# Optimization experiments

Measured on AMD Instinct MI355X. Metric: run time of the kernel, lower is better.

The kernel has to match this reference:

```python
import jax, jax.numpy as jnp
import numpy as np

N_HEADS = 8
N_HEAD_CH = 32
N_GROUPS = 8
NC = N_HEADS * N_HEAD_CH          # 256
GC = NC // N_GROUPS               # 32 group channels
OFFSET_RANGE_FACTOR = 2.0


def _layer_norm(x, w, b, eps=1e-5):
    mu = jnp.mean(x, -1, keepdims=True)
    var = jnp.var(x, -1, keepdims=True)
    return (x - mu) * jax.lax.rsqrt(var + eps) * w + b


def _conv2dmod(x, style, W):
    # StyleGAN2-style modulated 1x1 conv (lucidrains Conv2DMod, demod=True).
    # x (B,Ci,H,W), style (B,Ci), W (Co,Ci)
    w = W[None] * (style[:, None, :] + 1.0)                      # (B,Co,Ci)
    d = jax.lax.rsqrt(jnp.sum(w * w, axis=2, keepdims=True) + 1e-8)
    w = w * d
    return jnp.einsum('boi,bihw->bohw', w, x)


def _dwconv3x3(x, w, b):
    # depthwise 3x3, stride 1, pad 1; w (C,1,3,3)
    out = jax.lax.conv_general_dilated(
        x, w, window_strides=(1, 1), padding=[(1, 1), (1, 1)],
        dimension_numbers=('NCHW', 'OIHW', 'NCHW'),
        feature_group_count=x.shape[1])
    return out + b[None, :, None, None]


def _grid_sample(img, grid):
    # bilinear, align_corners=True, padding_mode='zeros'
    # img (N,C,H,W), grid (N,Hg,Wg,2) in xy order, values in ~[-1,1]
    N, C, H, W = img.shape
    gx = (grid[..., 0] + 1.0) * 0.5 * (W - 1)
    gy = (grid[..., 1] + 1.0) * 0.5 * (H - 1)
    x0 = jnp.floor(gx); y0 = jnp.floor(gy)
    wx1 = gx - x0; wy1 = gy - y0

    def gather(ix, iy):
        valid = ((ix >= 0) & (ix <= W - 1) & (iy >= 0) & (iy <= H - 1)).astype(img.dtype)
        ixc = jnp.clip(ix, 0, W - 1).astype(jnp.int32)
        iyc = jnp.clip(iy, 0, H - 1).astype(jnp.int32)
        vals = jax.vmap(lambda im, yy, xx: im[:, yy, xx])(img, iyc, ixc)  # (N,C,Hg,Wg)
        return vals * valid[:, None]

    x1 = x0 + 1.0; y1 = y0 + 1.0
    return (gather(x0, y0) * ((1 - wx1) * (1 - wy1))[:, None]
            + gather(x1, y0) * (wx1 * (1 - wy1))[:, None]
            + gather(x0, y1) * ((1 - wx1) * wy1)[:, None]
            + gather(x1, y1) * (wx1 * wy1)[:, None])


def _ref_points(Hk, Wk, BG, dtype):
    ry = jnp.linspace(0.5, Hk - 0.5, Hk, dtype=dtype) / (Hk - 1.0) * 2.0 - 1.0
    rx = jnp.linspace(0.5, Wk - 0.5, Wk, dtype=dtype) / (Wk - 1.0) * 2.0 - 1.0
    ref = jnp.stack(jnp.meshgrid(ry, rx, indexing='ij'), -1)  # (Hk,Wk,2) yx
    return jnp.broadcast_to(ref[None], (BG, Hk, Wk, 2))


def setup_inputs() -> dict:
    key = jax.random.key(0)
    ks = jax.random.split(key, 16)
    s = 0.02
    inp = {
        'x': jax.random.normal(ks[0], (2, NC, 32, 32), jnp.float32),
        'q': jax.random.normal(ks[1], (8, 2048, NC), jnp.float32),
        'mask': (jax.random.uniform(ks[2], (8, 2048, 1)) > 0.2).astype(jnp.float32),
        'Wq': jax.random.normal(ks[3], (NC, NC), jnp.float32) * s,
        'bq': jnp.zeros((NC,), jnp.float32),
        'Wmod': jax.random.normal(ks[4], (NC, NC), jnp.float32),
        'dw_w': jax.random.normal(ks[5], (GC, 1, 3, 3), jnp.float32) * s,
        'dw_b': jnp.zeros((GC,), jnp.float32),
        'ln_w': jnp.ones((GC,), jnp.float32),
        'ln_b': jnp.zeros((GC,), jnp.float32),
        'off_w': jax.random.normal(ks[6], (2, GC), jnp.float32) * s,
        'Wk': jax.random.normal(ks[7], (NC, NC), jnp.float32) * s,
        'bk': jnp.zeros((NC,), jnp.float32),
        'Wv': jax.random.normal(ks[8], (NC, NC), jnp.float32) * s,
        'bv': jnp.zeros((NC,), jnp.float32),
        'Wo': jax.random.normal(ks[9], (NC, NC), jnp.float32) * s,
        'bo': jnp.zeros((NC,), jnp.float32),
    }
    return inp


def reference(x, q, mask, Wq, bq, Wmod, dw_w, dw_b, ln_w, ln_b, off_w,
              Wk, bk, Wv, bv, Wo, bo):
    rn = q.shape[0] // x.shape[0]
    B, L, C = q.shape
    H, W = x.shape[2], x.shape[3]

    # masked mean pooling of queries -> conditioning vector
    q_cond = jnp.sum(q * mask, axis=1) / (jnp.sum(mask, axis=1) + 1e-6)   # (B,C)
    q_cond = q_cond @ Wq.T + bq

    # tile reference features: 'ref_n c h w -> (rn ref_n) c h w'
    xr = jnp.tile(x, (rn, 1, 1, 1))                                       # (B,C,H,W)

    # modulated 1x1 conv, then per-group offset network
    q_t = _conv2dmod(xr, q_cond, Wmod)                                    # (B,C,H,W)
    q_off = q_t.reshape(B * N_GROUPS, GC, H, W)
    t = _dwconv3x3(q_off, dw_w, dw_b)
    t = jnp.transpose(t, (0, 2, 3, 1))
    t = _layer_norm(t, ln_w, ln_b)
    t = jax.nn.gelu(t, approximate=False)
    t = jnp.transpose(t, (0, 3, 1, 2))
    offset = jnp.einsum('oi,bihw->bohw', off_w, t)                        # (BG,2,Hk,Wk)

    Hk, Wk_ = offset.shape[2], offset.shape[3]
    n_sample = Hk * Wk_
    offset_range = jnp.array([1.0 / (Hk - 1.0), 1.0 / (Wk_ - 1.0)],
                             dtype=x.dtype).reshape(1, 2, 1, 1)
    offset = jnp.tanh(offset) * offset_range * OFFSET_RANGE_FACTOR
    offset = jnp.transpose(offset, (0, 2, 3, 1))                          # (BG,Hk,Wk,2) yx

    ref = _ref_points(Hk, Wk_, B * N_GROUPS, x.dtype)
    pos = offset + ref                                                    # no clamp (orf>=0)

    # deformable gather
    xs = _grid_sample(xr.reshape(B * N_GROUPS, GC, H, W), pos[..., ::-1]) # (BG,GC,Hk,Wk)
    xs = xs.reshape(B, C, 1, n_sample)

    k = (jnp.einsum('oi,bimn->bomn', Wk, xs) + bk[None, :, None, None]
         ).reshape(B * N_HEADS, N_HEAD_CH, n_sample)
    v = (jnp.einsum('oi,bimn->bomn', Wv, xs) + bv[None, :, None, None]
         ).reshape(B * N_HEADS, N_HEAD_CH, n_sample)
    qh = jnp.transpose(q, (0, 2, 1)).reshape(B * N_HEADS, N_HEAD_CH, L)

    scale = N_HEAD_CH ** (-0.5)
    attn = jnp.einsum('bcm,bcn->bmn', qh, k) * scale                      # (BH,L,ns)
    # NOTE: source's attn.masked_fill(...) is non-in-place and discarded -> no mask here
    attn = jax.nn.softmax(attn, axis=2)
    out = jnp.einsum('bmn,bcn->bcm', attn, v)                             # (BH,hc,L)

    # '(b gn) c l -> b l (gn c)' with gn = n_groups (== n_heads)
    out = out.reshape(B, N_GROUPS, N_HEAD_CH, L).transpose(0, 3, 1, 2).reshape(B, L, NC)
    y = out @ Wo.T + bo
    return (y,
            pos.reshape(B, N_GROUPS, Hk, Wk_, 2),
            ref.reshape(B, N_GROUPS, Hk, Wk_, 2))
```

## Files before the change

kernel.cpp:

```cpp
#include <hip/hip_runtime.h>
#include <math.h>

typedef unsigned int uint;
typedef unsigned short ushort;
typedef __attribute__((ext_vector_type(8))) short short8;
typedef __attribute__((ext_vector_type(4))) float f32x4;

constexpr int CB  = 8;
constexpr int CL  = 2048;
constexpr int CC  = 256;
constexpr int CHC = 32;
constexpr int CGC = 32;
constexpr int CHW = 1024;
constexpr int CNS = 1024;
constexpr int CBG = 64;

constexpr size_t WS_QCOND = 2176;
constexpr size_t WS_WMOD  = 4224;
constexpr size_t WS_XT    = 266368;
constexpr size_t WS_QT    = 528512;
constexpr size_t WS_XST   = 2756736;
constexpr size_t WS_KB    = 3805312;
constexpr size_t WS_VB    = 4853888;
constexpr size_t WS_WB    = 5902464;
constexpr size_t WS_TMPB  = 6000768;
constexpr size_t WS_QB    = 8097920;
constexpr size_t WS_PART  = 10195072;
constexpr size_t WS_MPART = 10260608;

static __device__ __forceinline__ ushort f2bf(float f) {
  uint u = __float_as_uint(f);
  return (ushort)((u + 0x7FFFu + ((u >> 16) & 1u)) >> 16);
}
static __device__ __forceinline__ float bf2f(ushort u) {
  return __uint_as_float((uint)u << 16);
}
static __device__ __forceinline__ uint pack2bf(float a, float b) {
  return (uint)f2bf(a) | ((uint)f2bf(b) << 16);
}
static __device__ __forceinline__ uint packtrunc(float lo, float hi) {
  return __builtin_amdgcn_perm(__float_as_uint(hi), __float_as_uint(lo), 0x07060302u);
}

__global__ void k_pool(const float* __restrict__ q, const float* __restrict__ mask,
                       float* __restrict__ part, float* __restrict__ mpart,
                       ushort* __restrict__ qb) {
  int b  = blockIdx.x >> 5;
  int lc = blockIdx.x & 31;
  int l0 = lc * 64;
  int tid = threadIdx.x;
  const float scale = 0.17677669529663687f * 1.4426950408889634f;
  __shared__ float mloc[64];
  if (tid < 64) mloc[tid] = mask[b * CL + l0 + tid];
  __syncthreads();
  if (tid == 0) {
    float s = 0.f;
    for (int j = 0; j < 64; j++) s += mloc[j];
    mpart[b * 32 + lc] = s;
  }
  float acc = 0.f;
  const float* qp = q + (size_t)(b * CL + l0) * CC + tid;
  ushort* qw = qb + (size_t)(b * CL + l0) * CC + tid;
  for (int j = 0; j < 64; j++) {
    float v = qp[(size_t)j * CC];
    acc += v * mloc[j];
    qw[(size_t)j * CC] = f2bf(v * scale);
  }
  part[((size_t)(b * 32 + lc)) * CC + tid] = acc;
}

__global__ void k_qcond(const float* __restrict__ part, const float* __restrict__ mpart,
                        const float* __restrict__ Wq, const float* __restrict__ bq,
                        float* __restrict__ qcond) {
  int b = blockIdx.x, o = threadIdx.x;
  __shared__ float qm[CC];
  __shared__ float ms;
  float s = 0.f;
  const float* pp = part + (size_t)b * 32 * CC + o;
  #pragma unroll
  for (int lc = 0; lc < 32; lc++) s += pp[(size_t)lc * CC];
  if (o < 32) {
    float m = mpart[b * 32 + o];
    #pragma unroll
    for (int k = 1; k < 32; k <<= 1) m += __shfl_xor(m, k, 32);
    if (o == 0) ms = m;
  }
  __syncthreads();
  float inv = 1.f / (ms + 1e-6f);
  qm[o] = s * inv;
  __syncthreads();
  float acc = bq[o];
  const float* wrow = Wq + (size_t)o * CC;
  for (int i = 0; i < CC; i++) acc += wrow[i] * qm[i];
  qcond[b * CC + o] = acc;
}

__global__ void k_wprep(const float* __restrict__ Wmod, const float* __restrict__ qcond,
                        ushort* __restrict__ wmodb) {
  int b  = blockIdx.x >> 4;
  int og = blockIdx.x & 15;
  int tid = threadIdx.x;
  int ol = tid >> 4, seg = tid & 15;
  int o = og * 16 + ol;
  const float* wr = Wmod + (size_t)o * CC + seg * 16;
  const float* qc = qcond + b * CC + seg * 16;
  float m[16];
  float ss = 0.f;
  #pragma unroll
  for (int j = 0; j < 16; j++) {
    float v = wr[j] * (qc[j] + 1.f);
    m[j] = v;
    ss += v * v;
  }
  #pragma unroll
  for (int k = 1; k < 16; k <<= 1) ss += __shfl_xor(ss, k, 16);
  float d = rsqrtf(ss + 1e-8f);
  uint u[8];
  #pragma unroll
  for (int j = 0; j < 8; j++) u[j] = pack2bf(m[2 * j] * d, m[2 * j + 1] * d);
  ushort* dst = wmodb + ((size_t)(b * CC + o)) * CC + seg * 16;
  *(uint4*)(dst)     = make_uint4(u[0], u[1], u[2], u[3]);
  *(uint4*)(dst + 8) = make_uint4(u[4], u[5], u[6], u[7]);
}

__global__ void k_prep(const float* __restrict__ x, const float* __restrict__ Wk,
                       const float* __restrict__ Wv, const float* __restrict__ Wo,
                       ushort* __restrict__ xt, ushort* __restrict__ wb) {
  int bid = blockIdx.x;
  int tid = threadIdx.x;
  if (bid < 128) {
    int ref  = bid >> 6;
    int cblk = (bid >> 4) & 3;
    int hwblk = bid & 15;
    __shared__ float t[64][65];
    int c0 = cblk * 64, hw0 = hwblk * 64;
    const float* src = x + (size_t)ref * CC * CHW;
    int hl = tid & 63, cq = tid >> 6;
    #pragma unroll
    for (int r = 0; r < 16; r++) {
      int cl = cq * 16 + r;
      t[cl][hl] = src[(size_t)(c0 + cl) * CHW + hw0 + hl];
    }
    __syncthreads();
    int cl2 = tid & 63, hq = tid >> 6;
    #pragma unroll
    for (int r = 0; r < 16; r++) {
      int hwl = hq * 16 + r;
      xt[((size_t)(ref * CHW + hw0 + hwl)) * CC + c0 + cl2] = f2bf(t[cl2][hwl]);
    }
  } else {
    int t = (bid - 128) * 256 + tid;
    int which = t >> 13;
    size_t off = ((size_t)(t & 8191)) * 8;
    const float* src = (which == 0) ? Wk : (which == 1) ? Wv : Wo;
    float4 a = *(const float4*)(src + off);
    float4 b = *(const float4*)(src + off + 4);
    uint4 r;
    r.x = pack2bf(a.x, a.y); r.y = pack2bf(a.z, a.w);
    r.z = pack2bf(b.x, b.y); r.w = pack2bf(b.z, b.w);
    *(uint4*)(wb + (size_t)which * 65536 + off) = r;
  }
}

__launch_bounds__(256)
__global__ void k_mod_mfma(const ushort* __restrict__ wmodb, const ushort* __restrict__ xt,
                           float* __restrict__ qt) {
  int tid = threadIdx.x;
  int wid = tid >> 6, lane = tid & 63;
  int widx = blockIdx.x * 4 + wid;
  int b   = widx >> 10;
  int ot  = (widx >> 6) & 15;
  int hwt = widx & 63;
  int col = lane & 15, g = lane >> 4;
  int O0 = ot * 16, HW0 = hwt * 16;
  const ushort* ap = wmodb + ((size_t)(b * CC + O0 + col)) * CC + g * 8;
  const ushort* bp = xt + ((size_t)((b & 1) * CHW + HW0 + col)) * CC + g * 8;
  f32x4 acc = {0.f, 0.f, 0.f, 0.f};
  #pragma unroll
  for (int ks = 0; ks < 8; ks++) {
    short8 af = *(const short8*)(ap + ks * 32);
    short8 bf = *(const short8*)(bp + ks * 32);
    acc = __builtin_amdgcn_mfma_f32_16x16x32_bf16(af, bf, acc, 0, 0, 0);
  }
  float4 st;
  st.x = acc[0]; st.y = acc[1]; st.z = acc[2]; st.w = acc[3];
  *(float4*)(qt + ((size_t)(b * CHW + HW0 + col)) * CC + O0 + g * 4) = st;
}

__global__ void k_off_sample(const float* __restrict__ qt, const float* __restrict__ dww,
                             const float* __restrict__ dwb, const float* __restrict__ lnw,
                             const float* __restrict__ lnb, const float* __restrict__ offw,
                             const ushort* __restrict__ xt,
                             float* __restrict__ out_pos, float* __restrict__ out_ref,
                             ushort* __restrict__ xst) {
  int bg   = blockIdx.x >> 7;
  int pblk = blockIdx.x & 127;
  int tid  = threadIdx.x;
  int c = tid & 31, pp = tid >> 5;
  int p0 = pblk * 8;
  int yy = p0 >> 5;
  int xx = (p0 & 31) + pp;
  int p  = p0 + pp;
  const float* src = qt + ((size_t)(bg >> 3) * CHW) * CC + (bg & 7) * CGC + c;
  float acc = dwb[c];
  #pragma unroll
  for (int ky = 0; ky < 3; ky++) {
    int yr = yy + ky - 1;
    if (yr < 0 || yr > 31) continue;
    #pragma unroll
    for (int kx = 0; kx < 3; kx++) {
      int xc = xx + kx - 1;
      if (xc < 0 || xc > 31) continue;
      acc += dww[c * 9 + ky * 3 + kx] * src[(size_t)(yr * 32 + xc) * CC];
    }
  }
  float s1 = acc, s2 = acc * acc;
  #pragma unroll
  for (int m = 1; m < 32; m <<= 1) { s1 += __shfl_xor(s1, m, 32); s2 += __shfl_xor(s2, m, 32); }
  float mu  = s1 * (1.f / 32.f);
  float var = s2 * (1.f / 32.f) - mu * mu;
  float tn  = (acc - mu) * rsqrtf(var + 1e-5f) * lnw[c] + lnb[c];
  float g   = 0.5f * tn * (1.f + erff(tn * 0.70710678118654752f));
  float sy = offw[c] * g, sx = offw[32 + c] * g;
  #pragma unroll
  for (int m = 1; m < 32; m <<= 1) { sy += __shfl_xor(sy, m, 32); sx += __shfl_xor(sx, m, 32); }

  float mine  = tanhf((c & 1) ? sx : sy);
  float other = __shfl_xor(mine, 1, 32);
  float ty = (c & 1) ? other : mine;
  float tx = (c & 1) ? mine : other;

  float refy = (0.5f + (float)yy) * (2.f / 31.f) - 1.f;
  float refx = (0.5f + (float)xx) * (2.f / 31.f) - 1.f;
  float py = ty * (2.f / 31.f) + refy;
  float px = tx * (2.f / 31.f) + refx;
  if (c < 2) {
    int oidx = bg * 2048 + p * 2 + c;
    out_pos[oidx] = (c == 0) ? py : px;
    out_ref[oidx] = (c == 0) ? refy : refx;
  }

  float gx = (px + 1.f) * 15.5f;
  float gy = (py + 1.f) * 15.5f;
  float x0f = floorf(gx), y0f = floorf(gy);
  float wx = gx - x0f, wy = gy - y0f;
  int ix0 = (int)x0f, iy0 = (int)y0f;
  const ushort* img = xt + (size_t)(((bg >> 3) & 1)) * CHW * CC + (bg & 7) * CGC + c;
  float sacc = 0.f;
  #pragma unroll
  for (int dy = 0; dy < 2; dy++) {
    int iy = iy0 + dy;
    if (iy < 0 || iy > 31) continue;
    float wyv = dy ? wy : 1.f - wy;
    #pragma unroll
    for (int dx = 0; dx < 2; dx++) {
      int ix = ix0 + dx;
      if (ix < 0 || ix > 31) continue;
      float wxv = dx ? wx : 1.f - wx;
      sacc += wyv * wxv * bf2f(img[(size_t)(iy * 32 + ix) * CC]);
    }
  }
  xst[((size_t)((bg >> 3) * CNS) + p) * CC + (bg & 7) * CGC + c] = f2bf(sacc);
}

__launch_bounds__(256)
__global__ void k_kv_mfma(const ushort* __restrict__ xst, const ushort* __restrict__ wkb,
                          const ushort* __restrict__ wvb, const float* __restrict__ bk,
                          const float* __restrict__ bv, ushort* __restrict__ kb,
                          ushort* __restrict__ vb) {
  int tid = threadIdx.x;
  int wid = tid >> 6, lane = tid & 63;
  int widx = blockIdx.x * 4 + wid;
  int b   = widx >> 8;
  int ntg = (widx >> 3) & 31;
  int otg = widx & 7;
  int col = lane & 15, g = lane >> 4;
  int N0 = ntg * 32, O0 = otg * 32;

  const ushort* xs0 = xst + ((size_t)(b * CNS + N0 + col)) * CC + g * 8;
  const ushort* xs1 = xs0 + (size_t)16 * CC;
  const ushort* wk0 = wkb + (size_t)(O0 + col) * CC + g * 8;
  const ushort* wk1 = wk0 + (size_t)16 * CC;
  const ushort* wv0 = wvb + (size_t)(O0 + col) * CC + g * 8;
  const ushort* wv1 = wv0 + (size_t)16 * CC;

  f32x4 ka[2][2], va[2][2];
  #pragma unroll
  for (int Y = 0; Y < 2; Y++) {
    float bvv = bv[O0 + Y * 16 + col];
    #pragma unroll
    for (int r = 0; r < 4; r++) {
      float bkv = bk[O0 + Y * 16 + g * 4 + r];
      ka[0][Y][r] = bkv; ka[1][Y][r] = bkv;
      va[0][Y][r] = bvv; va[1][Y][r] = bvv;
    }
  }

  #pragma unroll
  for (int ks = 0; ks < 8; ks++) {
    short8 xf0 = *(const short8*)(xs0 + ks * 32);
    short8 xf1 = *(const short8*)(xs1 + ks * 32);
    short8 kf0 = *(const short8*)(wk0 + ks * 32);
    short8 kf1 = *(const short8*)(wk1 + ks * 32);
    short8 vf0 = *(const short8*)(wv0 + ks * 32);
    short8 vf1 = *(const short8*)(wv1 + ks * 32);
    ka[0][0] = __builtin_amdgcn_mfma_f32_16x16x32_bf16(kf0, xf0, ka[0][0], 0, 0, 0);
    ka[0][1] = __builtin_amdgcn_mfma_f32_16x16x32_bf16(kf1, xf0, ka[0][1], 0, 0, 0);
    ka[1][0] = __builtin_amdgcn_mfma_f32_16x16x32_bf16(kf0, xf1, ka[1][0], 0, 0, 0);
    ka[1][1] = __builtin_amdgcn_mfma_f32_16x16x32_bf16(kf1, xf1, ka[1][1], 0, 0, 0);
    va[0][0] = __builtin_amdgcn_mfma_f32_16x16x32_bf16(xf0, vf0, va[0][0], 0, 0, 0);
    va[0][1] = __builtin_amdgcn_mfma_f32_16x16x32_bf16(xf0, vf1, va[0][1], 0, 0, 0);
    va[1][0] = __builtin_amdgcn_mfma_f32_16x16x32_bf16(xf1, vf0, va[1][0], 0, 0, 0);
    va[1][1] = __builtin_amdgcn_mfma_f32_16x16x32_bf16(xf1, vf1, va[1][1], 0, 0, 0);
  }

  #pragma unroll
  for (int X = 0; X < 2; X++)
    #pragma unroll
    for (int Y = 0; Y < 2; Y++) {
      int Oy = O0 + Y * 16, Nx = N0 + X * 16;
      {
        int hh = Oy >> 5;
        int c0 = (Oy & 31) + g * 4;
        uint2 w;
        w.x = pack2bf(ka[X][Y][0], ka[X][Y][1]);
        w.y = pack2bf(ka[X][Y][2], ka[X][Y][3]);
        *(uint2*)(kb + ((size_t)((b * 8 + hh) * CNS + Nx + col)) * CHC + c0) = w;
      }
      {
        int o = Oy + col;
        int hh = o >> 5;
        uint2 w;
        w.x = pack2bf(va[X][Y][0], va[X][Y][1]);
        w.y = pack2bf(va[X][Y][2], va[X][Y][3]);
        *(uint2*)(vb + ((size_t)((b * 8 + hh) * CHC + (o & 31))) * CNS + Nx + g * 4) = w;
      }
    }
}

__launch_bounds__(512, 4)
__global__ void k_attn_mfma(const ushort* __restrict__ qb, const ushort* __restrict__ kb,
                            const ushort* __restrict__ vb, ushort* __restrict__ tmpb) {
  int bh = blockIdx.x >> 3;
  int mb = blockIdx.x & 7;
  int b = bh >> 3, h = bh & 7;
  int tid = threadIdx.x;
  int wid = tid >> 6, lane = tid & 63;
  int col = lane & 15, g = lane >> 4;
  int mA = mb * 256 + wid * 32 + col;

  __shared__ ushort Kst[2][64 * 40];
  __shared__ ushort Vst[2][32 * 72];
  __shared__ ushort plds[8][2048];

  char* pwA = (char*)&plds[wid][0];
  char* pwB = (char*)&plds[wid][1024];
  int swz = (col & 7) << 4;
  int wb0 = col * 128 + g * 8;
  int rb0 = (col * 128 + g * 16) ^ swz;
  int rb1 = (col * 128 + 64 + g * 16) ^ swz;

  const ushort* qpA = qb + ((size_t)(b * CL + mA)) * CC + h * CHC + g * 8;
  short8 qfA = *(const short8*)qpA;
  short8 qfB = *(const short8*)(qpA + 16 * CC);

  const ushort* kglob = kb + (size_t)bh * 32768 + tid * 4;
  const ushort* vglob = vb + (size_t)bh * 32768 + (tid >> 4) * 1024 + (tid & 15) * 4;
  int kdst = (tid >> 3) * 40 + (tid & 7) * 4;
  int vdst = (tid >> 4) * 72 + (tid & 15) * 4;

  f32x4 oA0 = {0.f,0.f,0.f,0.f}, oA1 = {0.f,0.f,0.f,0.f};
  f32x4 oB0 = {0.f,0.f,0.f,0.f}, oB1 = {0.f,0.f,0.f,0.f};
  float lA = 0.f, lB = 0.f;

  {
    uint2 kx = *(const uint2*)(kglob);
    uint2 vx = *(const uint2*)(vglob);
    *(uint2*)&Kst[0][kdst] = kx;
    *(uint2*)&Vst[0][vdst] = vx;
  }
  __syncthreads();

  int cur = 0;
  for (int ch = 0; ch < 16; ch++) {
    uint2 kx, vx;
    if (ch < 15) {
      kx = *(const uint2*)(kglob + (ch + 1) * 2048);
      vx = *(const uint2*)(vglob + (ch + 1) * 64);
    }

    const ushort* Kc = &Kst[cur][0];
    const ushort* Vc = &Vst[cur][0];
    short8 kf0 = *(const short8*)(Kc + ( 0 + col) * 40 + g * 8);
    short8 kf1 = *(const short8*)(Kc + (16 + col) * 40 + g * 8);
    short8 kf2 = *(const short8*)(Kc + (32 + col) * 40 + g * 8);
    short8 kf3 = *(const short8*)(Kc + (48 + col) * 40 + g * 8);
    short8 vf00 = *(const short8*)(Vc + (col     ) * 72 +  0 + g * 8);
    short8 vf01 = *(const short8*)(Vc + (col     ) * 72 + 32 + g * 8);
    short8 vf10 = *(const short8*)(Vc + (col + 16) * 72 +  0 + g * 8);
    short8 vf11 = *(const short8*)(Vc + (col + 16) * 72 + 32 + g * 8);

    f32x4 zero = {0.f,0.f,0.f,0.f};
    f32x4 sA0 = __builtin_amdgcn_mfma_f32_16x16x32_bf16(kf0, qfA, zero, 0, 0, 0);
    f32x4 sA1 = __builtin_amdgcn_mfma_f32_16x16x32_bf16(kf1, qfA, zero, 0, 0, 0);
    f32x4 sA2 = __builtin_amdgcn_mfma_f32_16x16x32_bf16(kf2, qfA, zero, 0, 0, 0);
    f32x4 sA3 = __builtin_amdgcn_mfma_f32_16x16x32_bf16(kf3, qfA, zero, 0, 0, 0);
    f32x4 sB0 = __builtin_amdgcn_mfma_f32_16x16x32_bf16(kf0, qfB, zero, 0, 0, 0);
    f32x4 sB1 = __builtin_amdgcn_mfma_f32_16x16x32_bf16(kf1, qfB, zero, 0, 0, 0);
    f32x4 sB2 = __builtin_amdgcn_mfma_f32_16x16x32_bf16(kf2, qfB, zero, 0, 0, 0);
    f32x4 sB3 = __builtin_amdgcn_mfma_f32_16x16x32_bf16(kf3, qfB, zero, 0, 0, 0);

    {
      float ps = 0.f;
      #pragma unroll
      for (int f = 0; f < 4; f++) {
        f32x4 s = (f == 0) ? sA0 : (f == 1) ? sA1 : (f == 2) ? sA2 : sA3;
        float p0 = __builtin_amdgcn_exp2f(s[0]);
        float p1 = __builtin_amdgcn_exp2f(s[1]);
        float p2 = __builtin_amdgcn_exp2f(s[2]);
        float p3 = __builtin_amdgcn_exp2f(s[3]);
        ps += (p0 + p1) + (p2 + p3);
        *(uint2*)(pwA + ((wb0 + f * 32) ^ swz)) = make_uint2(packtrunc(p0, p1), packtrunc(p2, p3));
      }
      lA += ps;
    }
    {
      float ps = 0.f;
      #pragma unroll
      for (int f = 0; f < 4; f++) {
        f32x4 s = (f == 0) ? sB0 : (f == 1) ? sB1 : (f == 2) ? sB2 : sB3;
        float p0 = __builtin_amdgcn_exp2f(s[0]);
        float p1 = __builtin_amdgcn_exp2f(s[1]);
        float p2 = __builtin_amdgcn_exp2f(s[2]);
        float p3 = __builtin_amdgcn_exp2f(s[3]);
        ps += (p0 + p1) + (p2 + p3);
        *(uint2*)(pwB + ((wb0 + f * 32) ^ swz)) = make_uint2(packtrunc(p0, p1), packtrunc(p2, p3));
      }
      lB += ps;
    }

    short8 pfA0 = *(const short8*)(pwA + rb0);
    short8 pfA1 = *(const short8*)(pwA + rb1);
    short8 pfB0 = *(const short8*)(pwB + rb0);
    short8 pfB1 = *(const short8*)(pwB + rb1);

    oA0 = __builtin_amdgcn_mfma_f32_16x16x32_bf16(vf00, pfA0, oA0, 0, 0, 0);
    oA0 = __builtin_amdgcn_mfma_f32_16x16x32_bf16(vf01, pfA1, oA0, 0, 0, 0);
    oA1 = __builtin_amdgcn_mfma_f32_16x16x32_bf16(vf10, pfA0, oA1, 0, 0, 0);
    oA1 = __builtin_amdgcn_mfma_f32_16x16x32_bf16(vf11, pfA1, oA1, 0, 0, 0);
    oB0 = __builtin_amdgcn_mfma_f32_16x16x32_bf16(vf00, pfB0, oB0, 0, 0, 0);
    oB0 = __builtin_amdgcn_mfma_f32_16x16x32_bf16(vf01, pfB1, oB0, 0, 0, 0);
    oB1 = __builtin_amdgcn_mfma_f32_16x16x32_bf16(vf10, pfB0, oB1, 0, 0, 0);
    oB1 = __builtin_amdgcn_mfma_f32_16x16x32_bf16(vf11, pfB1, oB1, 0, 0, 0);

    if (ch < 15) {
      *(uint2*)&Kst[cur ^ 1][kdst] = kx;
      *(uint2*)&Vst[cur ^ 1][vdst] = vx;
    }
    __syncthreads();
    cur ^= 1;
  }

  lA += __shfl_xor(lA, 16); lA += __shfl_xor(lA, 32);
  lB += __shfl_xor(lB, 16); lB += __shfl_xor(lB, 32);
  float rlA = 1.f / lA, rlB = 1.f / lB;

  ushort* opA = tmpb + ((size_t)(b * CL + mA)) * CC + h * CHC;
  ushort* opB = opA + 16 * CC;
  {
    uint2 w0, w1;
    w0.x = pack2bf(oA0[0] * rlA, oA0[1] * rlA);
    w0.y = pack2bf(oA0[2] * rlA, oA0[3] * rlA);
    w1.x = pack2bf(oA1[0] * rlA, oA1[1] * rlA);
    w1.y = pack2bf(oA1[2] * rlA, oA1[3] * rlA);
    *(uint2*)(opA + g * 4) = w0;
    *(uint2*)(opA + 16 + g * 4) = w1;
  }
  {
    uint2 w0, w1;
    w0.x = pack2bf(oB0[0] * rlB, oB0[1] * rlB);
    w0.y = pack2bf(oB0[2] * rlB, oB0[3] * rlB);
    w1.x = pack2bf(oB1[0] * rlB, oB1[1] * rlB);
    w1.y = pack2bf(oB1[2] * rlB, oB1[3] * rlB);
    *(uint2*)(opB + g * 4) = w0;
    *(uint2*)(opB + 16 + g * 4) = w1;
  }
}

__launch_bounds__(256)
__global__ void k_yproj_mfma(const ushort* __restrict__ tmpb, const ushort* __restrict__ wob,
                             const float* __restrict__ bo, float* __restrict__ y) {
  int tid = threadIdx.x;
  int wid = tid >> 6, lane = tid & 63;
  int widx = blockIdx.x * 4 + wid;
  int rt2 = widx >> 1;
  int og = widx & 1;
  int col = lane & 15, g = lane >> 4;
  int R0 = rt2 * 32, O0 = og * 128;

  const ushort* ap0 = tmpb + ((size_t)(R0 + col)) * CC + g * 8;
  const ushort* ap1 = ap0 + (size_t)16 * CC;
  const ushort* bp = wob + (size_t)(O0 + col) * CC + g * 8;

  f32x4 acc[2][8];
  #pragma unroll
  for (int o4 = 0; o4 < 8; o4++) {
    float bb = bo[O0 + o4 * 16 + col];
    #pragma unroll
    for (int r = 0; r < 4; r++) { acc[0][o4][r] = bb; acc[1][o4][r] = bb; }
  }

  #pragma unroll
  for (int ks = 0; ks < 8; ks++) {
    short8 af0 = *(const short8*)(ap0 + ks * 32);
    short8 af1 = *(const short8*)(ap1 + ks * 32);
    #pragma unroll
    for (int o4 = 0; o4 < 8; o4++) {
      short8 bf = *(const short8*)(bp + (size_t)o4 * 16 * CC + ks * 32);
      acc[0][o4] = __builtin_amdgcn_mfma_f32_16x16x32_bf16(af0, bf, acc[0][o4], 0, 0, 0);
      acc[1][o4] = __builtin_amdgcn_mfma_f32_16x16x32_bf16(af1, bf, acc[1][o4], 0, 0, 0);
    }
  }

  #pragma unroll
  for (int rr = 0; rr < 2; rr++)
    #pragma unroll
    for (int o4 = 0; o4 < 8; o4++)
      #pragma unroll
      for (int r = 0; r < 4; r++)
        y[(size_t)(R0 + rr * 16 + g * 4 + r) * CC + O0 + o4 * 16 + col] = acc[rr][o4][r];
}

extern "C" void kernel_launch(void* const* d_in, const int* in_sizes, int n_in,
                              void* d_out, int out_size, void* d_ws, size_t ws_size,
                              hipStream_t stream) {
  const float* x    = (const float*)d_in[0];
  const float* q    = (const float*)d_in[1];
  const float* mask = (const float*)d_in[2];
  const float* Wq   = (const float*)d_in[3];
  const float* bq   = (const float*)d_in[4];
  const float* Wmod = (const float*)d_in[5];
  const float* dw_w = (const float*)d_in[6];
  const float* dw_b = (const float*)d_in[7];
  const float* ln_w = (const float*)d_in[8];
  const float* ln_b = (const float*)d_in[9];
  const float* offw = (const float*)d_in[10];
  const float* Wk   = (const float*)d_in[11];
  const float* bk   = (const float*)d_in[12];
  const float* Wv   = (const float*)d_in[13];
  const float* bv   = (const float*)d_in[14];
  const float* Wo   = (const float*)d_in[15];
  const float* bo   = (const float*)d_in[16];

  float* ws = (float*)d_ws;
  float* out = (float*)d_out;
  float* out_y   = out;
  float* out_pos = out + (size_t)CB * CL * CC;
  float* out_ref = out_pos + (size_t)CBG * CHW * 2;

  ushort* wmodb = (ushort*)(ws + WS_WMOD);
  ushort* xt    = (ushort*)(ws + WS_XT);
  float*  qt    = ws + WS_QT;
  ushort* xst   = (ushort*)(ws + WS_XST);
  ushort* kbuf  = (ushort*)(ws + WS_KB);
  ushort* vbuf  = (ushort*)(ws + WS_VB);
  ushort* wkb   = (ushort*)(ws + WS_WB);
  ushort* wvb   = wkb + 65536;
  ushort* wob   = wkb + 131072;
  ushort* tmpb  = (ushort*)(ws + WS_TMPB);
  ushort* qbuf  = (ushort*)(ws + WS_QB);
  float*  part  = ws + WS_PART;
  float*  mpart = ws + WS_MPART;

  k_pool<<<256, 256, 0, stream>>>(q, mask, part, mpart, qbuf);
  k_qcond<<<8, 256, 0, stream>>>(part, mpart, Wq, bq, ws + WS_QCOND);
  k_prep<<<224, 256, 0, stream>>>(x, Wk, Wv, Wo, xt, wkb);
  k_wprep<<<128, 256, 0, stream>>>(Wmod, ws + WS_QCOND, wmodb);
  k_mod_mfma<<<2048, 256, 0, stream>>>(wmodb, xt, qt);
  k_off_sample<<<8192, 256, 0, stream>>>(qt, dw_w, dw_b, ln_w, ln_b, offw, xt,
                                         out_pos, out_ref, xst);
  k_kv_mfma<<<512, 256, 0, stream>>>(xst, wkb, wvb, bk, bv, kbuf, vbuf);
  k_attn_mfma<<<512, 512, 0, stream>>>(qbuf, kbuf, vbuf, tmpb);
  k_yproj_mfma<<<256, 256, 0, stream>>>(tmpb, wob, bo, out_y);
}
```

Measured before the change: 132.0 us.

## Merge pool and prep kernels, store qt as bf16, double attention chunk size

```diff
diff --git a/kernel.cpp b/kernel.cpp
--- a/kernel.cpp
+++ b/kernel.cpp
@@ -42,31 +42,70 @@
   return __builtin_amdgcn_perm(__float_as_uint(hi), __float_as_uint(lo), 0x07060302u);
 }
 
-__global__ void k_pool(const float* __restrict__ q, const float* __restrict__ mask,
-                       float* __restrict__ part, float* __restrict__ mpart,
-                       ushort* __restrict__ qb) {
-  int b  = blockIdx.x >> 5;
-  int lc = blockIdx.x & 31;
-  int l0 = lc * 64;
+__global__ void k_poolprep(const float* __restrict__ q, const float* __restrict__ mask,
+                           float* __restrict__ part, float* __restrict__ mpart,
+                           ushort* __restrict__ qb,
+                           const float* __restrict__ x, const float* __restrict__ Wk,
+                           const float* __restrict__ Wv, const float* __restrict__ Wo,
+                           ushort* __restrict__ xt, ushort* __restrict__ wb) {
+  int bid = blockIdx.x;
   int tid = threadIdx.x;
-  const float scale = 0.17677669529663687f * 1.4426950408889634f;
-  __shared__ float mloc[64];
-  if (tid < 64) mloc[tid] = mask[b * CL + l0 + tid];
-  __syncthreads();
-  if (tid == 0) {
-    float s = 0.f;
-    for (int j = 0; j < 64; j++) s += mloc[j];
-    mpart[b * 32 + lc] = s;
-  }
-  float acc = 0.f;
-  const float* qp = q + (size_t)(b * CL + l0) * CC + tid;
-  ushort* qw = qb + (size_t)(b * CL + l0) * CC + tid;
-  for (int j = 0; j < 64; j++) {
-    float v = qp[(size_t)j * CC];
-    acc += v * mloc[j];
-    qw[(size_t)j * CC] = f2bf(v * scale);
-  }
-  part[((size_t)(b * 32 + lc)) * CC + tid] = acc;
+  __shared__ float shbuf[64 * 65];
+  if (bid < 256) {
+    int b  = bid >> 5;
+    int lc = bid & 31;
+    int l0 = lc * 64;
+    const float scale = 0.17677669529663687f * 1.4426950408889634f;
+    float* mloc = shbuf;
+    if (tid < 64) mloc[tid] = mask[b * CL + l0 + tid];
+    __syncthreads();
+    if (tid == 0) {
+      float s = 0.f;
+      for (int j = 0; j < 64; j++) s += mloc[j];
+      mpart[b * 32 + lc] = s;
+    }
+    float acc = 0.f;
+    const float* qp = q + (size_t)(b * CL + l0) * CC + tid;
+    ushort* qw = qb + (size_t)(b * CL + l0) * CC + tid;
+    for (int j = 0; j < 64; j++) {
+      float v = qp[(size_t)j * CC];
+      acc += v * mloc[j];
+      qw[(size_t)j * CC] = f2bf(v * scale);
+    }
+    part[((size_t)(b * 32 + lc)) * CC + tid] = acc;
+  } else if (bid < 384) {
+    int b2 = bid - 256;
+    int ref  = b2 >> 6;
+    int cblk = (b2 >> 4) & 3;
+    int hwblk = b2 & 15;
+    float (*t)[65] = (float(*)[65])shbuf;
+    int c0 = cblk * 64, hw0 = hwblk * 64;
+    const float* src = x + (size_t)ref * CC * CHW;
+    int hl = tid & 63, cq = tid >> 6;
+    #pragma unroll
+    for (int r = 0; r < 16; r++) {
+      int cl = cq * 16 + r;
+      t[cl][hl] = src[(size_t)(c0 + cl) * CHW + hw0 + hl];
+    }
+    __syncthreads();
+    int cl2 = tid & 63, hq = tid >> 6;
+    #pragma unroll
+    for (int r = 0; r < 16; r++) {
+      int hwl = hq * 16 + r;
+      xt[((size_t)(ref * CHW + hw0 + hwl)) * CC + c0 + cl2] = f2bf(t[cl2][hwl]);
+    }
+  } else {
+    int t2 = (bid - 384) * 256 + tid;
+    int which = t2 >> 13;
+    size_t off = ((size_t)(t2 & 8191)) * 8;
+    const float* src = (which == 0) ? Wk : (which == 1) ? Wv : Wo;
+    float4 a = *(const float4*)(src + off);
+    float4 b = *(const float4*)(src + off + 4);
+    uint4 r;
+    r.x = pack2bf(a.x, a.y); r.y = pack2bf(a.z, a.w);
+    r.z = pack2bf(b.x, b.y); r.w = pack2bf(b.z, b.w);
+    *(uint4*)(wb + (size_t)which * 65536 + off) = r;
+  }
 }
 
 __global__ void k_qcond(const float* __restrict__ part, const float* __restrict__ mpart,
@@ -123,48 +162,9 @@
   *(uint4*)(dst + 8) = make_uint4(u[4], u[5], u[6], u[7]);
 }
 
-__global__ void k_prep(const float* __restrict__ x, const float* __restrict__ Wk,
-                       const float* __restrict__ Wv, const float* __restrict__ Wo,
-                       ushort* __restrict__ xt, ushort* __restrict__ wb) {
-  int bid = blockIdx.x;
-  int tid = threadIdx.x;
-  if (bid < 128) {
-    int ref  = bid >> 6;
-    int cblk = (bid >> 4) & 3;
-    int hwblk = bid & 15;
-    __shared__ float t[64][65];
-    int c0 = cblk * 64, hw0 = hwblk * 64;
-    const float* src = x + (size_t)ref * CC * CHW;
-    int hl = tid & 63, cq = tid >> 6;
-    #pragma unroll
-    for (int r = 0; r < 16; r++) {
-      int cl = cq * 16 + r;
-      t[cl][hl] = src[(size_t)(c0 + cl) * CHW + hw0 + hl];
-    }
-    __syncthreads();
-    int cl2 = tid & 63, hq = tid >> 6;
-    #pragma unroll
-    for (int r = 0; r < 16; r++) {
-      int hwl = hq * 16 + r;
-      xt[((size_t)(ref * CHW + hw0 + hwl)) * CC + c0 + cl2] = f2bf(t[cl2][hwl]);
-    }
-  } else {
-    int t = (bid - 128) * 256 + tid;
-    int which = t >> 13;
-    size_t off = ((size_t)(t & 8191)) * 8;
-    const float* src = (which == 0) ? Wk : (which == 1) ? Wv : Wo;
-    float4 a = *(const float4*)(src + off);
-    float4 b = *(const float4*)(src + off + 4);
-    uint4 r;
-    r.x = pack2bf(a.x, a.y); r.y = pack2bf(a.z, a.w);
-    r.z = pack2bf(b.x, b.y); r.w = pack2bf(b.z, b.w);
-    *(uint4*)(wb + (size_t)which * 65536 + off) = r;
-  }
-}
-
 __launch_bounds__(256)
 __global__ void k_mod_mfma(const ushort* __restrict__ wmodb, const ushort* __restrict__ xt,
-                           float* __restrict__ qt) {
+                           ushort* __restrict__ qtb) {
   int tid = threadIdx.x;
   int wid = tid >> 6, lane = tid & 63;
   int widx = blockIdx.x * 4 + wid;
@@ -182,12 +182,13 @@
     short8 bf = *(const short8*)(bp + ks * 32);
     acc = __builtin_amdgcn_mfma_f32_16x16x32_bf16(af, bf, acc, 0, 0, 0);
   }
-  float4 st;
-  st.x = acc[0]; st.y = acc[1]; st.z = acc[2]; st.w = acc[3];
-  *(float4*)(qt + ((size_t)(b * CHW + HW0 + col)) * CC + O0 + g * 4) = st;
-}
-
-__global__ void k_off_sample(const float* __restrict__ qt, const float* __restrict__ dww,
+  uint2 st;
+  st.x = pack2bf(acc[0], acc[1]);
+  st.y = pack2bf(acc[2], acc[3]);
+  *(uint2*)(qtb + ((size_t)(b * CHW + HW0 + col)) * CC + O0 + g * 4) = st;
+}
+
+__global__ void k_off_sample(const ushort* __restrict__ qtb, const float* __restrict__ dww,
                              const float* __restrict__ dwb, const float* __restrict__ lnw,
                              const float* __restrict__ lnb, const float* __restrict__ offw,
                              const ushort* __restrict__ xt,
@@ -201,7 +202,7 @@
   int yy = p0 >> 5;
   int xx = (p0 & 31) + pp;
   int p  = p0 + pp;
-  const float* src = qt + ((size_t)(bg >> 3) * CHW) * CC + (bg & 7) * CGC + c;
+  const ushort* src = qtb + ((size_t)(bg >> 3) * CHW) * CC + (bg & 7) * CGC + c;
   float acc = dwb[c];
   #pragma unroll
   for (int ky = 0; ky < 3; ky++) {
@@ -211,7 +212,7 @@
     for (int kx = 0; kx < 3; kx++) {
       int xc = xx + kx - 1;
       if (xc < 0 || xc > 31) continue;
-      acc += dww[c * 9 + ky * 3 + kx] * src[(size_t)(yr * 32 + xc) * CC];
+      acc += dww[c * 9 + ky * 3 + kx] * bf2f(src[(size_t)(yr * 32 + xc) * CC]);
     }
   }
   float s1 = acc, s2 = acc * acc;
@@ -349,8 +350,8 @@
   int col = lane & 15, g = lane >> 4;
   int mA = mb * 256 + wid * 32 + col;
 
-  __shared__ ushort Kst[2][64 * 40];
-  __shared__ ushort Vst[2][32 * 72];
+  __shared__ ushort Kst[2][2][64 * 40];
+  __shared__ ushort Vst[2][2][32 * 72];
   __shared__ ushort plds[8][2048];
 
   char* pwA = (char*)&plds[wid][0];
@@ -374,88 +375,100 @@
   float lA = 0.f, lB = 0.f;
 
   {
-    uint2 kx = *(const uint2*)(kglob);
-    uint2 vx = *(const uint2*)(vglob);
-    *(uint2*)&Kst[0][kdst] = kx;
-    *(uint2*)&Vst[0][vdst] = vx;
+    uint2 k0 = *(const uint2*)(kglob);
+    uint2 k1 = *(const uint2*)(kglob + 2048);
+    uint2 v0 = *(const uint2*)(vglob);
+    uint2 v1 = *(const uint2*)(vglob + 64);
+    *(uint2*)&Kst[0][0][kdst] = k0;
+    *(uint2*)&Kst[0][1][kdst] = k1;
+    *(uint2*)&Vst[0][0][vdst] = v0;
+    *(uint2*)&Vst[0][1][vdst] = v1;
   }
   __syncthreads();
 
   int cur = 0;
-  for (int ch = 0; ch < 16; ch++) {
-    uint2 kx, vx;
-    if (ch < 15) {
-      kx = *(const uint2*)(kglob + (ch + 1) * 2048);
-      vx = *(const uint2*)(vglob + (ch + 1) * 64);
-    }
-
-    const ushort* Kc = &Kst[cur][0];
-    const ushort* Vc = &Vst[cur][0];
-    short8 kf0 = *(const short8*)(Kc + ( 0 + col) * 40 + g * 8);
-    short8 kf1 = *(const short8*)(Kc + (16 + col) * 40 + g * 8);
-    short8 kf2 = *(const short8*)(Kc + (32 + col) * 40 + g * 8);
-    short8 kf3 = *(const short8*)(Kc + (48 + col) * 40 + g * 8);
-    short8 vf00 = *(const short8*)(Vc + (col     ) * 72 +  0 + g * 8);
-    short8 vf01 = *(const short8*)(Vc + (col     ) * 72 + 32 + g * 8);
-    short8 vf10 = *(const short8*)(Vc + (col + 16) * 72 +  0 + g * 8);
-    short8 vf11 = *(const short8*)(Vc + (col + 16) * 72 + 32 + g * 8);
-
-    f32x4 zero = {0.f,0.f,0.f,0.f};
-    f32x4 sA0 = __builtin_amdgcn_mfma_f32_16x16x32_bf16(kf0, qfA, zero, 0, 0, 0);
-    f32x4 sA1 = __builtin_amdgcn_mfma_f32_16x16x32_bf16(kf1, qfA, zero, 0, 0, 0);
-    f32x4 sA2 = __builtin_amdgcn_mfma_f32_16x16x32_bf16(kf2, qfA, zero, 0, 0, 0);
-    f32x4 sA3 = __builtin_amdgcn_mfma_f32_16x16x32_bf16(kf3, qfA, zero, 0, 0, 0);
-    f32x4 sB0 = __builtin_amdgcn_mfma_f32_16x16x32_bf16(kf0, qfB, zero, 0, 0, 0);
-    f32x4 sB1 = __builtin_amdgcn_mfma_f32_16x16x32_bf16(kf1, qfB, zero, 0, 0, 0);
-    f32x4 sB2 = __builtin_amdgcn_mfma_f32_16x16x32_bf16(kf2, qfB, zero, 0, 0, 0);
-    f32x4 sB3 = __builtin_amdgcn_mfma_f32_16x16x32_bf16(kf3, qfB, zero, 0, 0, 0);
-
-    {
-      float ps = 0.f;
-      #pragma unroll
-      for (int f = 0; f < 4; f++) {
-        f32x4 s = (f == 0) ? sA0 : (f == 1) ? sA1 : (f == 2) ? sA2 : sA3;
-        float p0 = __builtin_amdgcn_exp2f(s[0]);
-        float p1 = __builtin_amdgcn_exp2f(s[1]);
-        float p2 = __builtin_amdgcn_exp2f(s[2]);
-        float p3 = __builtin_amdgcn_exp2f(s[3]);
-        ps += (p0 + p1) + (p2 + p3);
-        *(uint2*)(pwA + ((wb0 + f * 32) ^ swz)) = make_uint2(packtrunc(p0, p1), packtrunc(p2, p3));
+  for (int it = 0; it < 8; it++) {
+    uint2 kx0, kx1, vx0, vx1;
+    if (it < 7) {
+      int cb = (it + 1) * 2;
+      kx0 = *(const uint2*)(kglob + (size_t)cb * 2048);
+      kx1 = *(const uint2*)(kglob + (size_t)(cb + 1) * 2048);
+      vx0 = *(const uint2*)(vglob + (size_t)cb * 64);
+      vx1 = *(const uint2*)(vglob + (size_t)(cb + 1) * 64);
+    }
+
+    #pragma unroll
+    for (int s = 0; s < 2; s++) {
+      const ushort* Kc = &Kst[cur][s][0];
+      const ushort* Vc = &Vst[cur][s][0];
+      short8 kf0 = *(const short8*)(Kc + ( 0 + col) * 40 + g * 8);
+      short8 kf1 = *(const short8*)(Kc + (16 + col) * 40 + g * 8);
+      short8 kf2 = *(const short8*)(Kc + (32 + col) * 40 + g * 8);
+      short8 kf3 = *(const short8*)(Kc + (48 + col) * 40 + g * 8);
+      short8 vf00 = *(const short8*)(Vc + (col     ) * 72 +  0 + g * 8);
+      short8 vf01 = *(const short8*)(Vc + (col     ) * 72 + 32 + g * 8);
+      short8 vf10 = *(const short8*)(Vc + (col + 16) * 72 +  0 + g * 8);
+      short8 vf11 = *(const short8*)(Vc + (col + 16) * 72 + 32 + g * 8);
+
+      f32x4 zero = {0.f,0.f,0.f,0.f};
+      f32x4 sA0 = __builtin_amdgcn_mfma_f32_16x16x32_bf16(kf0, qfA, zero, 0, 0, 0);
+      f32x4 sA1 = __builtin_amdgcn_mfma_f32_16x16x32_bf16(kf1, qfA, zero, 0, 0, 0);
+      f32x4 sA2 = __builtin_amdgcn_mfma_f32_16x16x32_bf16(kf2, qfA, zero, 0, 0, 0);
+      f32x4 sA3 = __builtin_amdgcn_mfma_f32_16x16x32_bf16(kf3, qfA, zero, 0, 0, 0);
+      f32x4 sB0 = __builtin_amdgcn_mfma_f32_16x16x32_bf16(kf0, qfB, zero, 0, 0, 0);
+      f32x4 sB1 = __builtin_amdgcn_mfma_f32_16x16x32_bf16(kf1, qfB, zero, 0, 0, 0);
+      f32x4 sB2 = __builtin_amdgcn_mfma_f32_16x16x32_bf16(kf2, qfB, zero, 0, 0, 0);
+      f32x4 sB3 = __builtin_amdgcn_mfma_f32_16x16x32_bf16(kf3, qfB, zero, 0, 0, 0);
+
+      {
+        float ps = 0.f;
+        #pragma unroll
+        for (int f = 0; f < 4; f++) {
+          f32x4 sv = (f == 0) ? sA0 : (f == 1) ? sA1 : (f == 2) ? sA2 : sA3;
+          float p0 = __builtin_amdgcn_exp2f(sv[0]);
+          float p1 = __builtin_amdgcn_exp2f(sv[1]);
+          float p2 = __builtin_amdgcn_exp2f(sv[2]);
+          float p3 = __builtin_amdgcn_exp2f(sv[3]);
+          ps += (p0 + p1) + (p2 + p3);
+          *(uint2*)(pwA + ((wb0 + f * 32) ^ swz)) = make_uint2(packtrunc(p0, p1), packtrunc(p2, p3));
+        }
+        lA += ps;
       }
-      lA += ps;
-    }
-    {
-      float ps = 0.f;
-      #pragma unroll
-      for (int f = 0; f < 4; f++) {
-        f32x4 s = (f == 0) ? sB0 : (f == 1) ? sB1 : (f == 2) ? sB2 : sB3;
-        float p0 = __builtin_amdgcn_exp2f(s[0]);
-        float p1 = __builtin_amdgcn_exp2f(s[1]);
-        float p2 = __builtin_amdgcn_exp2f(s[2]);
-        float p3 = __builtin_amdgcn_exp2f(s[3]);
-        ps += (p0 + p1) + (p2 + p3);
-        *(uint2*)(pwB + ((wb0 + f * 32) ^ swz)) = make_uint2(packtrunc(p0, p1), packtrunc(p2, p3));
+      {
+        float ps = 0.f;
+        #pragma unroll
+        for (int f = 0; f < 4; f++) {
+          f32x4 sv = (f == 0) ? sB0 : (f == 1) ? sB1 : (f == 2) ? sB2 : sB3;
+          float p0 = __builtin_amdgcn_exp2f(sv[0]);
+          float p1 = __builtin_amdgcn_exp2f(sv[1]);
+          float p2 = __builtin_amdgcn_exp2f(sv[2]);
+          float p3 = __builtin_amdgcn_exp2f(sv[3]);
+          ps += (p0 + p1) + (p2 + p3);
+          *(uint2*)(pwB + ((wb0 + f * 32) ^ swz)) = make_uint2(packtrunc(p0, p1), packtrunc(p2, p3));
+        }
+        lB += ps;
       }
-      lB += ps;
-    }
-
-    short8 pfA0 = *(const short8*)(pwA + rb0);
-    short8 pfA1 = *(const short8*)(pwA + rb1);
-    short8 pfB0 = *(const short8*)(pwB + rb0);
-    short8 pfB1 = *(const short8*)(pwB + rb1);
-
-    oA0 = __builtin_amdgcn_mfma_f32_16x16x32_bf16(vf00, pfA0, oA0, 0, 0, 0);
-    oA0 = __builtin_amdgcn_mfma_f32_16x16x32_bf16(vf01, pfA1, oA0, 0, 0, 0);
-    oA1 = __builtin_amdgcn_mfma_f32_16x16x32_bf16(vf10, pfA0, oA1, 0, 0, 0);
-    oA1 = __builtin_amdgcn_mfma_f32_16x16x32_bf16(vf11, pfA1, oA1, 0, 0, 0);
-    oB0 = __builtin_amdgcn_mfma_f32_16x16x32_bf16(vf00, pfB0, oB0, 0, 0, 0);
-    oB0 = __builtin_amdgcn_mfma_f32_16x16x32_bf16(vf01, pfB1, oB0, 0, 0, 0);
-    oB1 = __builtin_amdgcn_mfma_f32_16x16x32_bf16(vf10, pfB0, oB1, 0, 0, 0);
-    oB1 = __builtin_amdgcn_mfma_f32_16x16x32_bf16(vf11, pfB1, oB1, 0, 0, 0);
-
-    if (ch < 15) {
-      *(uint2*)&Kst[cur ^ 1][kdst] = kx;
-      *(uint2*)&Vst[cur ^ 1][vdst] = vx;
+
+      short8 pfA0 = *(const short8*)(pwA + rb0);
+      short8 pfA1 = *(const short8*)(pwA + rb1);
+      short8 pfB0 = *(const short8*)(pwB + rb0);
+      short8 pfB1 = *(const short8*)(pwB + rb1);
+
+      oA0 = __builtin_amdgcn_mfma_f32_16x16x32_bf16(vf00, pfA0, oA0, 0, 0, 0);
+      oA0 = __builtin_amdgcn_mfma_f32_16x16x32_bf16(vf01, pfA1, oA0, 0, 0, 0);
+      oA1 = __builtin_amdgcn_mfma_f32_16x16x32_bf16(vf10, pfA0, oA1, 0, 0, 0);
+      oA1 = __builtin_amdgcn_mfma_f32_16x16x32_bf16(vf11, pfA1, oA1, 0, 0, 0);
+      oB0 = __builtin_amdgcn_mfma_f32_16x16x32_bf16(vf00, pfB0, oB0, 0, 0, 0);
+      oB0 = __builtin_amdgcn_mfma_f32_16x16x32_bf16(vf01, pfB1, oB0, 0, 0, 0);
+      oB1 = __builtin_amdgcn_mfma_f32_16x16x32_bf16(vf10, pfB0, oB1, 0, 0, 0);
+      oB1 = __builtin_amdgcn_mfma_f32_16x16x32_bf16(vf11, pfB1, oB1, 0, 0, 0);
+    }
+
+    if (it < 7) {
+      *(uint2*)&Kst[cur ^ 1][0][kdst] = kx0;
+      *(uint2*)&Kst[cur ^ 1][1][kdst] = kx1;
+      *(uint2*)&Vst[cur ^ 1][0][vdst] = vx0;
+      *(uint2*)&Vst[cur ^ 1][1][vdst] = vx1;
     }
     __syncthreads();
     cur ^= 1;
@@ -560,7 +573,7 @@
 
   ushort* wmodb = (ushort*)(ws + WS_WMOD);
   ushort* xt    = (ushort*)(ws + WS_XT);
-  float*  qt    = ws + WS_QT;
+  ushort* qtb   = (ushort*)(ws + WS_QT);
   ushort* xst   = (ushort*)(ws + WS_XST);
   ushort* kbuf  = (ushort*)(ws + WS_KB);
   ushort* vbuf  = (ushort*)(ws + WS_VB);
@@ -572,12 +585,11 @@
   float*  part  = ws + WS_PART;
   float*  mpart = ws + WS_MPART;
 
-  k_pool<<<256, 256, 0, stream>>>(q, mask, part, mpart, qbuf);
+  k_poolprep<<<480, 256, 0, stream>>>(q, mask, part, mpart, qbuf, x, Wk, Wv, Wo, xt, wkb);
   k_qcond<<<8, 256, 0, stream>>>(part, mpart, Wq, bq, ws + WS_QCOND);
-  k_prep<<<224, 256, 0, stream>>>(x, Wk, Wv, Wo, xt, wkb);
   k_wprep<<<128, 256, 0, stream>>>(Wmod, ws + WS_QCOND, wmodb);
-  k_mod_mfma<<<2048, 256, 0, stream>>>(wmodb, xt, qt);
-  k_off_sample<<<8192, 256, 0, stream>>>(qt, dw_w, dw_b, ln_w, ln_b, offw, xt,
+  k_mod_mfma<<<2048, 256, 0, stream>>>(wmodb, xt, qtb);
+  k_off_sample<<<8192, 256, 0, stream>>>(qtb, dw_w, dw_b, ln_w, ln_b, offw, xt,
                                          out_pos, out_ref, xst);
   k_kv_mfma<<<512, 256, 0, stream>>>(xst, wkb, wvb, bk, bv, kbuf, vbuf);
   k_attn_mfma<<<512, 512, 0, stream>>>(qbuf, kbuf, vbuf, tmpb);
```

Measured after the change: 126.6 us, median of 2. 1.04x faster.
